# Optimization experiments

Hardware: AMD Instinct MI355X
Metric: run time of the kernel (lower is better)

## Reference

```python
import jax, jax.numpy as jnp
import numpy as np

B, T, D, H, R = 64, 128, 128, 128, 4  # num_T == num_H == num_D forced by shape consistency
E = D * R  # SwiGLU expansion dim
EPS = 1e-5


def _pswiglu(x, Wu, bu, Wg, bg, Wd, bd):
    # x: [B,T,D]; per-token independent SwiGLU MLPs batched as one einsum
    up = jnp.einsum('btd,tde->bte', x, Wu) + bu          # [B,T,E]
    gate = jax.nn.silu(jnp.einsum('btd,tde->bte', x, Wg) + bg)
    return jnp.einsum('bte,ted->btd', up * gate, Wd) + bd  # [B,T,D]


def _rmsnorm(x, scale):
    rms = jnp.sqrt(jnp.mean(x * x, axis=-1, keepdims=True) + EPS)
    return x / rms * scale


def _token_mix(x, nT, nD, nH):
    # reshape (B,nT,nD)->(B,nT,nH,dk), transpose, merge -> (B,nH,nT*dk)
    dk = nD // nH
    b = x.shape[0]
    return x.reshape(b, nT, nH, dk).transpose(0, 2, 1, 3).reshape(b, nH, nT * dk)


def setup_inputs() -> dict:
    key = jax.random.key(0)
    ks = jax.random.split(key, 7)
    s = 0.02
    return {
        'x': jax.random.normal(ks[0], (B, T, D), dtype=jnp.float32),
        'W1_up': jax.random.normal(ks[1], (T, D, E), dtype=jnp.float32) * s,
        'b1_up': jnp.zeros((T, E), jnp.float32),
        'W1_gate': jax.random.normal(ks[2], (T, D, E), dtype=jnp.float32) * s,
        'b1_gate': jnp.zeros((T, E), jnp.float32),
        'W1_down': jax.random.normal(ks[3], (T, E, D), dtype=jnp.float32) * s,
        'b1_down': jnp.zeros((T, D), jnp.float32),
        'scale1': jnp.ones((D,), jnp.float32),
        'W2_up': jax.random.normal(ks[4], (T, D, E), dtype=jnp.float32) * s,
        'b2_up': jnp.zeros((T, E), jnp.float32),
        'W2_gate': jax.random.normal(ks[5], (T, D, E), dtype=jnp.float32) * s,
        'b2_gate': jnp.zeros((T, E), jnp.float32),
        'W2_down': jax.random.normal(ks[6], (T, E, D), dtype=jnp.float32) * s,
        'b2_down': jnp.zeros((T, D), jnp.float32),
        'scale2': jnp.ones((D,), jnp.float32),
    }


def reference(x, W1_up, b1_up, W1_gate, b1_gate, W1_down, b1_down, scale1,
              W2_up, b2_up, W2_gate, b2_gate, W2_down, b2_down, scale2):
    mixed = _token_mix(x, T, D, H)                         # [B,H,T*D/H] == [B,N,N]
    x1 = _rmsnorm(mixed + _pswiglu(mixed, W1_up, b1_up, W1_gate, b1_gate, W1_down, b1_down), scale1)
    rev = _token_mix(x1, T, H, D)                          # revert transpose
    out = _rmsnorm(rev + _pswiglu(rev, W2_up, b2_up, W2_gate, b2_gate, W2_down, b2_down), scale2)
    return out
```

## Files before the change

kernel.cpp:

```cpp
#include <hip/hip_runtime.h>

typedef __bf16 bf16x8 __attribute__((ext_vector_type(8)));
typedef float f32x4 __attribute__((ext_vector_type(4)));
typedef unsigned int uint;

#define XA_STR 152

union Frag { __bf16 b[8]; bf16x8 v; unsigned short u[8]; };

__device__ __forceinline__ unsigned short bfbits(float f) {
  union { __bf16 h; unsigned short s; } c; c.h = (__bf16)f; return c.s;
}
__device__ __forceinline__ float bf2f(unsigned short h) {
  return __uint_as_float(((uint)h) << 16);
}

#define GLOAD4(dst, voff, base) \
  asm volatile("global_load_dwordx4 %0, %1, %2" : "=v"(dst) : "v"(voff), "s"(base))
#define GLOAD4I(dst, voff, base, IMM) \
  asm volatile("global_load_dwordx4 %0, %1, %2 offset:" #IMM : "=v"(dst) : "v"(voff), "s"(base))
#define GLOAD1(dst, voff, base) \
  asm volatile("global_load_dword %0, %1, %2" : "=v"(dst) : "v"(voff), "s"(base))
#define WAITV(N) asm volatile("s_waitcnt vmcnt(" #N ")" ::: "memory")
#define BARX()   asm volatile("s_waitcnt lgkmcnt(0)\n\ts_barrier" ::: "memory")

template <typename T>
__global__ __launch_bounds__(256) void transpose_in(const T* __restrict__ src,
                                                    unsigned short* __restrict__ dst) {
  __shared__ unsigned short tile[64][68];
  const int b  = blockIdx.x >> 2;
  const int f0 = ((blockIdx.x >> 1) & 1) * 64;
  const int s0 = (blockIdx.x & 1) * 64;
  const int j = threadIdx.x & 63, i0 = threadIdx.x >> 6;
  const T* sp = src + b * 16384 + f0 * 128 + s0 + j;
#pragma unroll
  for (int p = 0; p < 16; ++p) {
    const int i = i0 + p * 4;
    if constexpr (sizeof(T) == 4) tile[i][j] = bfbits((float)sp[i * 128]);
    else                          tile[i][j] = (unsigned short)sp[i * 128];
  }
  __syncthreads();
  unsigned short* dp = dst + s0 * 8192 + b * 128 + f0 + j;
#pragma unroll
  for (int p = 0; p < 16; ++p) {
    const int i = i0 + p * 4;
    dp[(size_t)i * 8192] = tile[j][i];
  }
}

__global__ __launch_bounds__(512, 4) void mlp_main(
    const unsigned short* __restrict__ Xt,
    const float* __restrict__ Wu, const float* __restrict__ bu,
    const float* __restrict__ Wg, const float* __restrict__ bg,
    const float* __restrict__ Wd,
    unsigned short* __restrict__ partial)
{
  const int bid = blockIdx.x;
  const int s = bid >> 2, q = bid & 3;
  const int tid = threadIdx.x;
  const int wv = tid >> 6, lane = tid & 63;
  const int l16 = lane & 15, lg = lane >> 4;
  const int col = wv * 16 + l16;

  __shared__ __align__(16) float SU[32 * 128];
  __shared__ __align__(16) float SG[32 * 128];
  __shared__ __align__(16) unsigned short xa[64 * XA_STR];

  const float* WuS = Wu + (size_t)s * 65536 + q * 128;
  const float* WgS = Wg + (size_t)s * 65536 + q * 128;
  const float* WdS = Wd + (size_t)s * 65536 + (size_t)q * 16384;
  const float* buS = bu + s * 512 + q * 128;
  const float* bgS = bg + s * 512 + q * 128;
  const unsigned short* XtS = Xt + (size_t)s * 8192;

  uint vuo = (uint)((4 * wv + 2 + (lane >> 5)) * 2048 + (lane & 31) * 16);
  uint vdo = (uint)((4 * wv + (lane >> 5)) * 512 + (lane & 31) * 16);
  const uint vbo = (uint)(col * 4);
  const uint vx0 = (uint)(tid * 16), vx1 = vx0 + 8192;

  f32x4 uq[3][2], gq[3][2], dq[4][2];
  f32x4 xq0, xq1;
  float buv, bgv;

#define ISSUE_U(SET) do { \
    GLOAD4I(uq[SET][0], vuo, WuS, -4096); GLOAD4(uq[SET][1], vuo, WuS); \
    GLOAD4I(gq[SET][0], vuo, WgS, -4096); GLOAD4(gq[SET][1], vuo, WgS); \
    vuo += 65536; } while (0)
#define ISSUE_D(SET) do { \
    GLOAD4(dq[SET][0], vdo, WdS); GLOAD4I(dq[SET][1], vdo, WdS, 1024); \
    vdo += 16384; } while (0)

  GLOAD4(xq0, vx0, XtS);
  GLOAD4(xq1, vx1, XtS);
  GLOAD1(buv, vbo, buS);
  GLOAD1(bgv, vbo, bgS);
  ISSUE_U(0); ISSUE_U(1); ISSUE_U(2);

  WAITV(12);
  {
    const int m0 = tid >> 4, ch0 = tid & 15;
    *(f32x4*)&xa[m0 * XA_STR + (ch0 << 3)] = xq0;
    const int p1 = tid + 512, m1 = p1 >> 4, ch1 = p1 & 15;
    *(f32x4*)&xa[m1 * XA_STR + (ch1 << 3)] = xq1;
  }
  BARX();

  const int wsA = (4 * wv + (lane >> 5)) * 128 + (lane & 31) * 4;
  const int wsB = wsA + 256;

  Frag a[4];
#define LOADA(KK) do { \
    _Pragma("unroll") \
    for (int mt = 0; mt < 4; ++mt) \
      a[mt].v = *(const bf16x8*)&xa[(mt * 16 + l16) * XA_STR + (((KK) * 4 + lg) << 3)]; \
  } while (0)

#define BF(f, SL) do { \
    const float* bp = (SL) + (lg * 8) * 128 + col; \
    _Pragma("unroll") \
    for (int j = 0; j < 8; ++j) f.b[j] = (__bf16)bp[j * 128]; } while (0)

  f32x4 au[4] = {}, ag[4] = {}, ad[4] = {};
#define MFMA4(f, acc) do { \
    _Pragma("unroll") \
    for (int mt = 0; mt < 4; ++mt) \
      acc[mt] = __builtin_amdgcn_mfma_f32_16x16x32_bf16(a[mt].v, f.v, acc[mt], 0, 0, 0); \
  } while (0)

#define UP_STEP(SET, KK, ISSUE_STMT) do { \
    BARX();  \
    *(f32x4*)&SU[wsA] = uq[SET][0]; *(f32x4*)&SU[wsB] = uq[SET][1]; \
    *(f32x4*)&SG[wsA] = gq[SET][0]; *(f32x4*)&SG[wsB] = gq[SET][1]; \
    ISSUE_STMT; \
    BARX();  \
    LOADA(KK); \
    { Frag fu; BF(fu, SU); MFMA4(fu, au); } \
    { Frag fg; BF(fg, SG); MFMA4(fg, ag); } \
  } while (0)

  WAITV(8);  UP_STEP(0, 0, ISSUE_U(0));
  WAITV(8);  UP_STEP(1, 1, ISSUE_D(0));
  WAITV(6);  UP_STEP(2, 2, ISSUE_D(1));
  WAITV(4);  UP_STEP(0, 3, ISSUE_D(2));

  float a2v[4][4];
#pragma unroll
  for (int mt = 0; mt < 4; ++mt)
#pragma unroll
    for (int r = 0; r < 4; ++r) {
      const float uv = au[mt][r] + buv;
      const float gv = ag[mt][r] + bgv;
      a2v[mt][r] = uv * (gv / (1.f + __expf(-gv)));
    }
  BARX();
#pragma unroll
  for (int mt = 0; mt < 4; ++mt)
#pragma unroll
    for (int r = 0; r < 4; ++r)
      xa[(mt * 16 + lg * 4 + r) * XA_STR + col] = bfbits(a2v[mt][r]);
  ISSUE_D(3);

#define DN_STEP(SET, KK) do { \
    BARX(); \
    *(f32x4*)&SU[wsA] = dq[SET][0]; *(f32x4*)&SU[wsB] = dq[SET][1]; \
    BARX(); \
    LOADA(KK); \
    { Frag fd; BF(fd, SU); MFMA4(fd, ad); } \
  } while (0)

  WAITV(6);  DN_STEP(0, 0);
  WAITV(4);  DN_STEP(1, 1);
  WAITV(2);  DN_STEP(2, 2);
  WAITV(0);  DN_STEP(3, 3);

  unsigned short* po = partial + (size_t)bid * 8192;
#pragma unroll
  for (int mt = 0; mt < 4; ++mt)
#pragma unroll
    for (int r = 0; r < 4; ++r)
      po[(mt * 16 + lg * 4 + r) * 128 + col] = bfbits(ad[mt][r]);

#undef ISSUE_U
#undef ISSUE_D
#undef LOADA
#undef BF
#undef MFMA4
#undef UP_STEP
#undef DN_STEP
}

template <typename TO>
__global__ __launch_bounds__(256) void finish(
    const unsigned short* __restrict__ part, const unsigned short* __restrict__ xt,
    const float* __restrict__ bd, const float* __restrict__ scale,
    TO* __restrict__ y)
{
  const int s = blockIdx.x >> 1, half = blockIdx.x & 1;
  const int wvt = threadIdx.x >> 6, lane = threadIdx.x & 63;
  const int d0 = lane * 2;
  const float sc0 = scale[d0], sc1 = scale[d0 + 1];
  const float b0 = bd[s * 128 + d0], b1 = bd[s * 128 + d0 + 1];
  const unsigned short* pb = part + (size_t)s * 4 * 8192;
  const unsigned short* xb = xt + (size_t)s * 8192;
  for (int i = 0; i < 8; ++i) {
    const int b = half * 32 + i * 4 + wvt;
    const uint rx = *(const uint*)(xb + b * 128 + d0);
    float z0 = b0 + bf2f((unsigned short)rx);
    float z1 = b1 + bf2f((unsigned short)(rx >> 16));
#pragma unroll
    for (int p = 0; p < 4; ++p) {
      const uint rp = *(const uint*)(pb + p * 8192 + b * 128 + d0);
      z0 += bf2f((unsigned short)rp);
      z1 += bf2f((unsigned short)(rp >> 16));
    }
    float ss = z0 * z0 + z1 * z1;
#pragma unroll
    for (int off = 32; off; off >>= 1) ss += __shfl_xor(ss, off);
    const float inv = rsqrtf(ss * (1.f / 128.f) + 1e-5f);
    if constexpr (sizeof(TO) == 4) {
      float2 o = make_float2(z0 * inv * sc0, z1 * inv * sc1);
      *(float2*)((float*)y + (size_t)b * 16384 + s * 128 + d0) = o;
    } else {
      const uint o = (uint)bfbits(z0 * inv * sc0) | ((uint)bfbits(z1 * inv * sc1) << 16);
      *(uint*)((unsigned short*)y + (size_t)b * 16384 + s * 128 + d0) = o;
    }
  }
}

extern "C" void kernel_launch(void* const* d_in, const int* in_sizes, int n_in,
                              void* d_out, int out_size, void* d_ws, size_t ws_size,
                              hipStream_t stream) {
  (void)in_sizes; (void)n_in; (void)out_size; (void)ws_size;
  const float* x   = (const float*)d_in[0];
  const float* W1u = (const float*)d_in[1];
  const float* b1u = (const float*)d_in[2];
  const float* W1g = (const float*)d_in[3];
  const float* b1g = (const float*)d_in[4];
  const float* W1d = (const float*)d_in[5];
  const float* b1d = (const float*)d_in[6];
  const float* sc1 = (const float*)d_in[7];
  const float* W2u = (const float*)d_in[8];
  const float* b2u = (const float*)d_in[9];
  const float* W2g = (const float*)d_in[10];
  const float* b2g = (const float*)d_in[11];
  const float* W2d = (const float*)d_in[12];
  const float* b2d = (const float*)d_in[13];
  const float* sc2 = (const float*)d_in[14];
  float* out = (float*)d_out;

  unsigned short* xt   = (unsigned short*)d_ws;
  unsigned short* y1   = xt + (size_t)1048576;
  unsigned short* part = y1 + (size_t)1048576;

  transpose_in<float><<<256, 256, 0, stream>>>(x, xt);
  mlp_main<<<512, 512, 0, stream>>>(xt, W1u, b1u, W1g, b1g, W1d, part);
  finish<unsigned short><<<256, 256, 0, stream>>>(part, xt, b1d, sc1, y1);
  transpose_in<unsigned short><<<256, 256, 0, stream>>>(y1, xt);
  mlp_main<<<512, 512, 0, stream>>>(xt, W2u, b2u, W2g, b2g, W2d, part);
  finish<float><<<256, 256, 0, stream>>>(part, xt, b2d, sc2, out);
}
```

Measured before the change: 66.73 us.

## Load weight fragments directly into registers, dropping LDS staging and barriers

Weight tiles were loaded as dwordx4, staged through shared memory (SU/SG) and then gathered per lane for MFMA B fragments. Now each lane issues scalar dword loads straight into the 8 registers of its B fragment, with a three-deep register prefetch schedule. This removes the LDS round trip and most of the per-step barriers. In exchange it issues many narrower global loads, each a 64-byte-row gather per wave, and uses more VGPRs, which may hurt coalescing or occupancy.

```diff
diff --git a/kernel.cpp b/kernel.cpp
--- a/kernel.cpp
+++ b/kernel.cpp
@@ -15,14 +15,13 @@
   return __uint_as_float(((uint)h) << 16);
 }
 
-#define GLOAD4(dst, voff, base) \
+#define GL1(dst, voff, base, IMM) \
+  asm volatile("global_load_dword %0, %1, %2 offset:" #IMM : "=v"(dst) : "v"(voff), "s"(base))
+#define GL4(dst, voff, base) \
   asm volatile("global_load_dwordx4 %0, %1, %2" : "=v"(dst) : "v"(voff), "s"(base))
-#define GLOAD4I(dst, voff, base, IMM) \
-  asm volatile("global_load_dwordx4 %0, %1, %2 offset:" #IMM : "=v"(dst) : "v"(voff), "s"(base))
-#define GLOAD1(dst, voff, base) \
-  asm volatile("global_load_dword %0, %1, %2" : "=v"(dst) : "v"(voff), "s"(base))
-#define WAITV(N) asm volatile("s_waitcnt vmcnt(" #N ")" ::: "memory")
-#define BARX()   asm volatile("s_waitcnt lgkmcnt(0)\n\ts_barrier" ::: "memory")
+#define WAITV(N) do { asm volatile("s_waitcnt vmcnt(" #N ")" ::: "memory"); \
+  __builtin_amdgcn_sched_barrier(0); } while (0)
+#define BARX() asm volatile("s_waitcnt lgkmcnt(0)\n\ts_barrier" ::: "memory")
 
 template <typename T>
 __global__ __launch_bounds__(256) void transpose_in(const T* __restrict__ src,
@@ -62,41 +61,76 @@
   const int l16 = lane & 15, lg = lane >> 4;
   const int col = wv * 16 + l16;
 
-  __shared__ __align__(16) float SU[32 * 128];
-  __shared__ __align__(16) float SG[32 * 128];
   __shared__ __align__(16) unsigned short xa[64 * XA_STR];
 
-  const float* WuS = Wu + (size_t)s * 65536 + q * 128;
-  const float* WgS = Wg + (size_t)s * 65536 + q * 128;
-  const float* WdS = Wd + (size_t)s * 65536 + (size_t)q * 16384;
-  const float* buS = bu + s * 512 + q * 128;
-  const float* bgS = bg + s * 512 + q * 128;
+  const float* WuS = Wu + (size_t)s * 65536;
+  const float* WgS = Wg + (size_t)s * 65536;
+  const float* WdS = Wd + (size_t)s * 65536;
   const unsigned short* XtS = Xt + (size_t)s * 8192;
 
-  uint vuo = (uint)((4 * wv + 2 + (lane >> 5)) * 2048 + (lane & 31) * 16);
-  uint vdo = (uint)((4 * wv + (lane >> 5)) * 512 + (lane & 31) * 16);
-  const uint vbo = (uint)(col * 4);
+  uint vu = (uint)(((lg * 8) * 512 + q * 128 + col) * 4);
+  uint vd = (uint)(((q * 128 + lg * 8) * 128 + col) * 4);
+  const uint vbo = (uint)((q * 128 + col) * 4);
   const uint vx0 = (uint)(tid * 16), vx1 = vx0 + 8192;
 
-  f32x4 uq[3][2], gq[3][2], dq[4][2];
+  float u0[8], g0[8], u1[8], g1[8], u2[8], g2[8];
+  float d0[8], d1[8], d2[8], d3[8];
   f32x4 xq0, xq1;
   float buv, bgv;
 
-#define ISSUE_U(SET) do { \
-    GLOAD4I(uq[SET][0], vuo, WuS, -4096); GLOAD4(uq[SET][1], vuo, WuS); \
-    GLOAD4I(gq[SET][0], vuo, WgS, -4096); GLOAD4(gq[SET][1], vuo, WgS); \
-    vuo += 65536; } while (0)
-#define ISSUE_D(SET) do { \
-    GLOAD4(dq[SET][0], vdo, WdS); GLOAD4I(dq[SET][1], vdo, WdS, 1024); \
-    vdo += 16384; } while (0)
-
-  GLOAD4(xq0, vx0, XtS);
-  GLOAD4(xq1, vx1, XtS);
-  GLOAD1(buv, vbo, buS);
-  GLOAD1(bgv, vbo, bgS);
-  ISSUE_U(0); ISSUE_U(1); ISSUE_U(2);
-
-  WAITV(12);
+#define ISSUE_UG(U, G) do { \
+  GL1(U[0], vu, WuS, 0); GL1(U[1], vu, WuS, 2048); \
+  GL1(G[0], vu, WgS, 0); GL1(G[1], vu, WgS, 2048); vu += 4096; \
+  GL1(U[2], vu, WuS, 0); GL1(U[3], vu, WuS, 2048); \
+  GL1(G[2], vu, WgS, 0); GL1(G[3], vu, WgS, 2048); vu += 4096; \
+  GL1(U[4], vu, WuS, 0); GL1(U[5], vu, WuS, 2048); \
+  GL1(G[4], vu, WgS, 0); GL1(G[5], vu, WgS, 2048); vu += 4096; \
+  GL1(U[6], vu, WuS, 0); GL1(U[7], vu, WuS, 2048); \
+  GL1(G[6], vu, WgS, 0); GL1(G[7], vu, WgS, 2048); vu += 53248;  \
+} while (0)
+
+#define ISSUE_D(D) do { \
+  GL1(D[0], vd, WdS, 0);    GL1(D[1], vd, WdS, 512); \
+  GL1(D[2], vd, WdS, 1024); GL1(D[3], vd, WdS, 1536); \
+  GL1(D[4], vd, WdS, 2048); GL1(D[5], vd, WdS, 2560); \
+  GL1(D[6], vd, WdS, 3072); GL1(D[7], vd, WdS, 3584); vd += 16384; \
+} while (0)
+
+  Frag a[4];
+#define LOADA(KK) do { \
+  _Pragma("unroll") \
+  for (int mt = 0; mt < 4; ++mt) \
+    a[mt].v = *(const bf16x8*)&xa[(mt * 16 + l16) * XA_STR + (((KK) * 4 + lg) << 3)]; \
+} while (0)
+
+  f32x4 au[4] = {}, ag[4] = {}, ad[4] = {};
+#define STEP_UG(U, G) do { \
+  Frag fu, fg; \
+  _Pragma("unroll") \
+  for (int j = 0; j < 8; ++j) { fu.b[j] = (__bf16)U[j]; fg.b[j] = (__bf16)G[j]; } \
+  _Pragma("unroll") \
+  for (int mt = 0; mt < 4; ++mt) { \
+    au[mt] = __builtin_amdgcn_mfma_f32_16x16x32_bf16(a[mt].v, fu.v, au[mt], 0, 0, 0); \
+    ag[mt] = __builtin_amdgcn_mfma_f32_16x16x32_bf16(a[mt].v, fg.v, ag[mt], 0, 0, 0); } \
+} while (0)
+
+#define STEP_D(D) do { \
+  Frag fd; \
+  _Pragma("unroll") \
+  for (int j = 0; j < 8; ++j) fd.b[j] = (__bf16)D[j]; \
+  _Pragma("unroll") \
+  for (int mt = 0; mt < 4; ++mt) \
+    ad[mt] = __builtin_amdgcn_mfma_f32_16x16x32_bf16(a[mt].v, fd.v, ad[mt], 0, 0, 0); \
+} while (0)
+
+  GL4(xq0, vx0, XtS);
+  GL4(xq1, vx1, XtS);
+  GL1(buv, vbo, bu + s * 512, 0);
+  GL1(bgv, vbo, bg + s * 512, 0);
+  ISSUE_UG(u0, g0);
+  ISSUE_UG(u1, g1);
+
+  WAITV(32);
   {
     const int m0 = tid >> 4, ch0 = tid & 15;
     *(f32x4*)&xa[m0 * XA_STR + (ch0 << 3)] = xq0;
@@ -105,43 +139,14 @@
   }
   BARX();
 
-  const int wsA = (4 * wv + (lane >> 5)) * 128 + (lane & 31) * 4;
-  const int wsB = wsA + 256;
-
-  Frag a[4];
-#define LOADA(KK) do { \
-    _Pragma("unroll") \
-    for (int mt = 0; mt < 4; ++mt) \
-      a[mt].v = *(const bf16x8*)&xa[(mt * 16 + l16) * XA_STR + (((KK) * 4 + lg) << 3)]; \
-  } while (0)
-
-#define BF(f, SL) do { \
-    const float* bp = (SL) + (lg * 8) * 128 + col; \
-    _Pragma("unroll") \
-    for (int j = 0; j < 8; ++j) f.b[j] = (__bf16)bp[j * 128]; } while (0)
-
-  f32x4 au[4] = {}, ag[4] = {}, ad[4] = {};
-#define MFMA4(f, acc) do { \
-    _Pragma("unroll") \
-    for (int mt = 0; mt < 4; ++mt) \
-      acc[mt] = __builtin_amdgcn_mfma_f32_16x16x32_bf16(a[mt].v, f.v, acc[mt], 0, 0, 0); \
-  } while (0)
-
-#define UP_STEP(SET, KK, ISSUE_STMT) do { \
-    BARX();  \
-    *(f32x4*)&SU[wsA] = uq[SET][0]; *(f32x4*)&SU[wsB] = uq[SET][1]; \
-    *(f32x4*)&SG[wsA] = gq[SET][0]; *(f32x4*)&SG[wsB] = gq[SET][1]; \
-    ISSUE_STMT; \
-    BARX();  \
-    LOADA(KK); \
-    { Frag fu; BF(fu, SU); MFMA4(fu, au); } \
-    { Frag fg; BF(fg, SG); MFMA4(fg, ag); } \
-  } while (0)
-
-  WAITV(8);  UP_STEP(0, 0, ISSUE_U(0));
-  WAITV(8);  UP_STEP(1, 1, ISSUE_D(0));
-  WAITV(6);  UP_STEP(2, 2, ISSUE_D(1));
-  WAITV(4);  UP_STEP(0, 3, ISSUE_D(2));
+  ISSUE_UG(u2, g2);
+  WAITV(32); LOADA(0); STEP_UG(u0, g0);
+  ISSUE_UG(u0, g0);
+  WAITV(32); LOADA(1); STEP_UG(u1, g1);
+  ISSUE_D(d0);
+  WAITV(24); LOADA(2); STEP_UG(u2, g2);
+  ISSUE_D(d1);
+  WAITV(16); LOADA(3); STEP_UG(u0, g0);
 
   float a2v[4][4];
 #pragma unroll
@@ -158,20 +163,14 @@
 #pragma unroll
     for (int r = 0; r < 4; ++r)
       xa[(mt * 16 + lg * 4 + r) * XA_STR + col] = bfbits(a2v[mt][r]);
-  ISSUE_D(3);
-
-#define DN_STEP(SET, KK) do { \
-    BARX(); \
-    *(f32x4*)&SU[wsA] = dq[SET][0]; *(f32x4*)&SU[wsB] = dq[SET][1]; \
-    BARX(); \
-    LOADA(KK); \
-    { Frag fd; BF(fd, SU); MFMA4(fd, ad); } \
-  } while (0)
-
-  WAITV(6);  DN_STEP(0, 0);
-  WAITV(4);  DN_STEP(1, 1);
-  WAITV(2);  DN_STEP(2, 2);
-  WAITV(0);  DN_STEP(3, 3);
+  ISSUE_D(d2);
+  BARX();
+
+  ISSUE_D(d3);
+  WAITV(24); LOADA(0); STEP_D(d0);
+  WAITV(16); LOADA(1); STEP_D(d1);
+  WAITV(8);  LOADA(2); STEP_D(d2);
+  WAITV(0);  LOADA(3); STEP_D(d3);
 
   unsigned short* po = partial + (size_t)bid * 8192;
 #pragma unroll
@@ -180,13 +179,11 @@
     for (int r = 0; r < 4; ++r)
       po[(mt * 16 + lg * 4 + r) * 128 + col] = bfbits(ad[mt][r]);
 
-#undef ISSUE_U
+#undef ISSUE_UG
 #undef ISSUE_D
 #undef LOADA
-#undef BF
-#undef MFMA4
-#undef UP_STEP
-#undef DN_STEP
+#undef STEP_UG
+#undef STEP_D
 }
 
 template <typename TO>
```

After: 61.94 us. -7.2%, faster.
